# Optimization experiments

Hardware: AMD Instinct MI355X
Metric: run time of the kernel (lower is better)

The kernel has to match this reference:

```python
import jax, jax.numpy as jnp
import numpy as np

N_STATE = 1280
N_HEAD = 20
D_HEAD = N_STATE // N_HEAD  # 64
N_MLP = 4 * N_STATE         # 5120
EPS = 1e-5


def _layer_norm(x, gamma, beta):
    mu = jnp.mean(x, axis=-1, keepdims=True)
    var = jnp.mean(jnp.square(x - mu), axis=-1, keepdims=True)
    return (x - mu) * jax.lax.rsqrt(var + EPS) * gamma + beta


def setup_inputs() -> dict:
    key = jax.random.key(0)
    ks = jax.random.split(key, 16)
    s = lambda fan_in: 1.0 / np.sqrt(fan_in)
    d = {
        "x": jax.random.normal(ks[0], (1, 1500, N_STATE), jnp.float32),
        # attention projections (stored [in, out]; torch Linear does x @ W.T + b)
        "Wq": jax.random.normal(ks[1], (N_STATE, N_STATE), jnp.float32) * s(N_STATE),
        "bq": jax.random.normal(ks[2], (N_STATE,), jnp.float32) * 0.02,
        "Wk": jax.random.normal(ks[3], (N_STATE, N_STATE), jnp.float32) * s(N_STATE),  # no bias
        "Wv": jax.random.normal(ks[4], (N_STATE, N_STATE), jnp.float32) * s(N_STATE),
        "bv": jax.random.normal(ks[5], (N_STATE,), jnp.float32) * 0.02,
        "Wo": jax.random.normal(ks[6], (N_STATE, N_STATE), jnp.float32) * s(N_STATE),
        "bo": jax.random.normal(ks[7], (N_STATE,), jnp.float32) * 0.02,
        # layer norms
        "ln1_g": jnp.ones((N_STATE,), jnp.float32),
        "ln1_b": jnp.zeros((N_STATE,), jnp.float32),
        "ln2_g": jnp.ones((N_STATE,), jnp.float32),
        "ln2_b": jnp.zeros((N_STATE,), jnp.float32),
        # MLP
        "W1": jax.random.normal(ks[8], (N_STATE, N_MLP), jnp.float32) * s(N_STATE),
        "b1": jax.random.normal(ks[9], (N_MLP,), jnp.float32) * 0.02,
        "W2": jax.random.normal(ks[10], (N_MLP, N_STATE), jnp.float32) * s(N_MLP),
        "b2": jax.random.normal(ks[11], (N_STATE,), jnp.float32) * 0.02,
    }
    return d


def reference(x, Wq, bq, Wk, Wv, bv, Wo, bo, ln1_g, ln1_b, ln2_g, ln2_b, W1, b1, W2, b2):
    B, S, C = x.shape
    scale = D_HEAD ** -0.5

    # --- multi-head self-attention ---
    h = _layer_norm(x, ln1_g, ln1_b)
    q = (h @ Wq + bq).reshape(B, S, N_HEAD, D_HEAD)
    k = (h @ Wk).reshape(B, S, N_HEAD, D_HEAD)
    v = (h @ Wv + bv).reshape(B, S, N_HEAD, D_HEAD)
    # scores: [B, H, Q, K]; softmax over keys (dim=1 'k' in the torch einsum)
    scores = jnp.einsum('bqhd,bkhd->bhqk', q, k) * scale
    w = jax.nn.softmax(scores, axis=-1)
    attn = jnp.einsum('bhqk,bkhd->bqhd', w, v).reshape(B, S, C)
    attn = attn @ Wo + bo
    x = x + attn

    # --- MLP (exact GELU, matching torch nn.GELU default) ---
    h2 = _layer_norm(x, ln2_g, ln2_b)
    h2 = jax.nn.gelu(h2 @ W1 + b1, approximate=False)
    x = x + (h2 @ W2 + b2)
    return x
```

## Files before the change

### kernel.cpp

```cpp
#include <hip/hip_runtime.h>
#include <hip/hip_bf16.h>
#include <math.h>

typedef __bf16 bf16x8 __attribute__((ext_vector_type(8)));
typedef float f32x4 __attribute__((ext_vector_type(4)));

#define SEQ 1500
#define CDIM 1280
#define NHEAD 20
#define DHEAD 64
#define NMLP 5120
#define QKVN 3840
#define VTLD 1504
#define APAD 68

#define GLOAD_LDS16(gp, lp)                                                    \
  __builtin_amdgcn_global_load_lds(                                            \
      (const __attribute__((address_space(1))) unsigned int*)(gp),             \
      (__attribute__((address_space(3))) unsigned int*)(lp), 16, 0, 0)

__global__ __launch_bounds__(256) void pack_params_kernel(
    const unsigned int* __restrict__ xw, const void* bq, const void* bv,
    const void* bo, const void* g1, const void* be1, const void* g2,
    const void* be2, const void* b1, const void* b2,
    __bf16* __restrict__ pb, int* __restrict__ flag) {
  __shared__ int cnt[256];
  const unsigned int w = xw[threadIdx.x];
  const unsigned int e = (w >> 7) & 0xFF;
  cnt[threadIdx.x] = (e >= 100 && e <= 150) ? 1 : 0;
  __syncthreads();
  for (int s = 128; s > 0; s >>= 1) {
    if (threadIdx.x < (unsigned)s) cnt[threadIdx.x] += cnt[threadIdx.x + s];
    __syncthreads();
  }
  const int isbf = (cnt[0] >= 160) ? 1 : 0;
  if (blockIdx.x == 0 && threadIdx.x == 0) flag[0] = isbf;
  const int i = blockIdx.x * 256 + threadIdx.x;
  if (i >= 16640) return;
  auto ld = [&](const void* p, int j) -> float {
    return isbf ? (float)((const __bf16*)p)[j] : ((const float*)p)[j];
  };
  float v;
  if (i < 3840) {
    if (i < 1280) v = ld(bq, i);
    else if (i < 2560) v = 0.f;
    else v = ld(bv, i - 2560);
  } else if (i < 5120) v = ld(bo, i - 3840);
  else if (i < 6400) v = ld(g1, i - 5120);
  else if (i < 7680) v = ld(be1, i - 6400);
  else if (i < 8960) v = ld(g2, i - 7680);
  else if (i < 10240) v = ld(be2, i - 8960);
  else if (i < 15360) v = ld(b1, i - 10240);
  else v = ld(b2, i - 15360);
  pb[i] = (__bf16)v;
}

__device__ __forceinline__ void transpose_body(const void* in, __bf16* out,
                                               int K, int N, int isbf,
                                               int bx, int by) {
  __shared__ __bf16 t[32][33];
  const int tx = threadIdx.x, ty = threadIdx.y;
  const int n0 = bx * 32, k0 = by * 32;
  if (isbf) {
    const __bf16* s = (const __bf16*)in;
#pragma unroll
    for (int i = ty; i < 32; i += 8)
      t[i][tx] = s[(size_t)(k0 + i) * N + n0 + tx];
  } else {
    const float* s = (const float*)in;
#pragma unroll
    for (int i = ty; i < 32; i += 8)
      t[i][tx] = (__bf16)s[(size_t)(k0 + i) * N + n0 + tx];
  }
  __syncthreads();
#pragma unroll
  for (int i = ty; i < 32; i += 8)
    out[(size_t)(n0 + i) * K + k0 + tx] = t[tx][i];
}

__global__ __launch_bounds__(256) void transpose_all_kernel(
    const void* Wq, const void* Wk, const void* Wv, const void* Wo,
    const void* W1, const void* W2, __bf16* __restrict__ Wqkvt,
    __bf16* __restrict__ Wot, __bf16* __restrict__ W1t,
    __bf16* __restrict__ W2t, const int* __restrict__ flag) {
  const int id = blockIdx.x;
  const int isbf = flag[0];
  if (id < 6400) {
    const int w = id / 1600, r = id % 1600;
    const void* in = (w == 0) ? Wq : (w == 1) ? Wk : (w == 2) ? Wv : Wo;
    __bf16* out = (w < 3) ? (Wqkvt + (size_t)w * CDIM * CDIM) : Wot;
    transpose_body(in, out, CDIM, CDIM, isbf, r % 40, r / 40);
  } else if (id < 12800) {
    const int r = id - 6400;
    transpose_body(W1, W1t, CDIM, NMLP, isbf, r % 160, r / 160);
  } else {
    const int r = id - 12800;
    transpose_body(W2, W2t, NMLP, CDIM, isbf, r % 40, r / 40);
  }
}

__global__ __launch_bounds__(256) void transpose_act_kernel(const __bf16* __restrict__ in,
                                                            __bf16* __restrict__ out,
                                                            int istride) {
  __shared__ __bf16 t[32][33];
  const int tx = threadIdx.x, ty = threadIdx.y;
  const int n0 = blockIdx.x * 32, k0 = blockIdx.y * 32;
#pragma unroll
  for (int i = ty; i < 32; i += 8) {
    const int k = k0 + i;
    t[i][tx] = (k < SEQ) ? in[(size_t)k * istride + n0 + tx] : (__bf16)0.f;
  }
  __syncthreads();
#pragma unroll
  for (int i = ty; i < 32; i += 8) {
    const int kk = k0 + tx;
    if (kk < VTLD) out[(size_t)(n0 + i) * VTLD + kk] = t[tx][i];
  }
}

__global__ __launch_bounds__(256) void ln_kernel(const void* __restrict__ X,
                                                 const __bf16* __restrict__ gamma,
                                                 const __bf16* __restrict__ beta,
                                                 __bf16* __restrict__ Y,
                                                 const int* __restrict__ flag) {
  const int isf32 = (flag[0] == 0);
  const int row = blockIdx.x;
  float v[5];
  float s = 0.f, s2 = 0.f;
#pragma unroll
  for (int i = 0; i < 5; ++i) {
    const int c = threadIdx.x + 256 * i;
    const size_t idx = (size_t)row * CDIM + c;
    v[i] = isf32 ? ((const float*)X)[idx] : (float)((const __bf16*)X)[idx];
    s += v[i];
    s2 += v[i] * v[i];
  }
  const int lane = threadIdx.x & 63, wv = threadIdx.x >> 6;
#pragma unroll
  for (int off = 32; off > 0; off >>= 1) {
    s += __shfl_down(s, off);
    s2 += __shfl_down(s2, off);
  }
  __shared__ float red[8];
  if (lane == 0) { red[wv] = s; red[4 + wv] = s2; }
  __syncthreads();
  s = red[0] + red[1] + red[2] + red[3];
  s2 = red[4] + red[5] + red[6] + red[7];
  const float mu = s * (1.f / CDIM);
  const float var = s2 * (1.f / CDIM) - mu * mu;
  const float rstd = rsqrtf(fmaxf(var, 0.f) + 1e-5f);
#pragma unroll
  for (int i = 0; i < 5; ++i) {
    const int c = threadIdx.x + 256 * i;
    Y[(size_t)row * CDIM + c] =
        (__bf16)((v[i] - mu) * rstd * (float)gamma[c] + (float)beta[c]);
  }
}

__global__ __launch_bounds__(256) void resid_ln_kernel(
    const float* __restrict__ P, const __bf16* __restrict__ bo,
    const void* __restrict__ X, const __bf16* __restrict__ gamma,
    const __bf16* __restrict__ beta, __bf16* __restrict__ X1,
    __bf16* __restrict__ H2, const int* __restrict__ flag) {
  const int isf32 = (flag[0] == 0);
  const int row = blockIdx.x;
  const int MN = SEQ * CDIM;
  float v[5];
  float s = 0.f, s2 = 0.f;
#pragma unroll
  for (int i = 0; i < 5; ++i) {
    const int c = threadIdx.x + 256 * i;
    const size_t idx = (size_t)row * CDIM + c;
    const float xv = isf32 ? ((const float*)X)[idx] : (float)((const __bf16*)X)[idx];
    const float val = P[idx] + P[MN + idx] + (float)bo[c] + xv;
    X1[idx] = (__bf16)val;
    v[i] = val;
    s += val;
    s2 += val * val;
  }
  const int lane = threadIdx.x & 63, wv = threadIdx.x >> 6;
#pragma unroll
  for (int off = 32; off > 0; off >>= 1) {
    s += __shfl_down(s, off);
    s2 += __shfl_down(s2, off);
  }
  __shared__ float red[8];
  if (lane == 0) { red[wv] = s; red[4 + wv] = s2; }
  __syncthreads();
  s = red[0] + red[1] + red[2] + red[3];
  s2 = red[4] + red[5] + red[6] + red[7];
  const float mu = s * (1.f / CDIM);
  const float var = s2 * (1.f / CDIM) - mu * mu;
  const float rstd = rsqrtf(fmaxf(var, 0.f) + 1e-5f);
#pragma unroll
  for (int i = 0; i < 5; ++i) {
    const int c = threadIdx.x + 256 * i;
    H2[(size_t)row * CDIM + c] =
        (__bf16)((v[i] - mu) * rstd * (float)gamma[c] + (float)beta[c]);
  }
}

__global__ __launch_bounds__(256) void gemm64_kernel(
    const __bf16* __restrict__ A, const __bf16* __restrict__ Bt,
    const __bf16* __restrict__ bias, void* __restrict__ Cv,
    int M, int N, int K, int KS, int gelu, int nsplit) {
  __shared__ __bf16 As[2][64 * 32];
  __shared__ __bf16 Bs[2][128 * 32];
  const int bm = blockIdx.x, bn = blockIdx.y, sz = blockIdx.z;
  const int tid = threadIdx.x;
  const int lane = tid & 63, wave = tid >> 6;
  const int l16 = lane & 15, kq = (lane >> 4) << 3;
  const int lrow = lane >> 2, lcol = (lane & 3) << 3;
  const int wn = wave * 32;

  f32x4 acc[4][2];
  const f32x4 zero = {0.f, 0.f, 0.f, 0.f};
#pragma unroll
  for (int i = 0; i < 4; ++i)
#pragma unroll
    for (int j = 0; j < 2; ++j) acc[i][j] = zero;

  const int kbeg = sz * KS;
  int kend = kbeg + KS;
  if (kend > K) kend = K;

  int ga = bm * 64 + wave * 16 + lrow;
  if (ga > M - 1) ga = M - 1;
  const __bf16* Ap = A + (size_t)ga * K + lcol;

  for (int k0 = kbeg; k0 < kend; k0 += 64) {
#pragma unroll
    for (int c = 0; c < 2; ++c)
      GLOAD_LDS16(Ap + k0 + c * 32, &As[c][wave * 512]);
#pragma unroll
    for (int c = 0; c < 2; ++c)
#pragma unroll
      for (int t = 0; t < 2; ++t) {
        const int seg = t * 4 + wave;
        const int gb = bn * 128 + seg * 16 + lrow;
        GLOAD_LDS16(Bt + (size_t)gb * K + k0 + c * 32 + lcol, &Bs[c][seg * 512]);
      }
    __syncthreads();
    bf16x8 af[4][2], bfr[2][2];
#pragma unroll
    for (int i = 0; i < 4; ++i)
#pragma unroll
      for (int c = 0; c < 2; ++c)
        af[i][c] = *(const bf16x8*)(&As[c][(i * 16 + l16) * 32 + kq]);
#pragma unroll
    for (int j = 0; j < 2; ++j)
#pragma unroll
      for (int c = 0; c < 2; ++c)
        bfr[j][c] = *(const bf16x8*)(&Bs[c][(wn + j * 16 + l16) * 32 + kq]);
#pragma unroll
    for (int i = 0; i < 4; ++i)
#pragma unroll
      for (int j = 0; j < 2; ++j)
#pragma unroll
        for (int c = 0; c < 2; ++c)
          acc[i][j] = __builtin_amdgcn_mfma_f32_16x16x32_bf16(af[i][c], bfr[j][c],
                                                              acc[i][j], 0, 0, 0);
    __syncthreads();
  }

  const int rq4 = (lane >> 4) * 4;
  if (nsplit > 1) {
    float* P = (float*)Cv + (size_t)sz * M * N;
#pragma unroll
    for (int i = 0; i < 4; ++i)
#pragma unroll
      for (int r = 0; r < 4; ++r) {
        const int grow = bm * 64 + i * 16 + rq4 + r;
        if (grow >= M) continue;
#pragma unroll
        for (int j = 0; j < 2; ++j) {
          const int gcol = bn * 128 + wn + j * 16 + l16;
          P[(size_t)grow * N + gcol] = acc[i][j][r];
        }
      }
  } else {
    __bf16* Cb = (__bf16*)Cv;
#pragma unroll
    for (int i = 0; i < 4; ++i)
#pragma unroll
      for (int r = 0; r < 4; ++r) {
        const int grow = bm * 64 + i * 16 + rq4 + r;
        if (grow >= M) continue;
#pragma unroll
        for (int j = 0; j < 2; ++j) {
          const int gcol = bn * 128 + wn + j * 16 + l16;
          float vv = acc[i][j][r];
          if (bias) vv += (float)bias[gcol];
          if (gelu) vv = 0.5f * vv * (1.f + erff(vv * 0.70710678118654752f));
          Cb[(size_t)grow * N + gcol] = (__bf16)vv;
        }
      }
  }
}

__global__ __launch_bounds__(512, 2) void gemm8ph_kernel(
    const __bf16* __restrict__ A, const __bf16* __restrict__ Bt,
    const __bf16* __restrict__ bias, __bf16* __restrict__ C,
    int M, int N, int K, int gelu, int mtiles) {
  __shared__ __bf16 As[2][128 * 64];
  __shared__ __bf16 Bs[2][256 * 64];

  const int nwg = mtiles * (N >> 8);
  const int qq = nwg >> 3, rr = nwg & 7;
  const int xcd = blockIdx.x & 7, rk = blockIdx.x >> 3;
  const int wg = (xcd < rr ? xcd * (qq + 1) : rr * (qq + 1) + (xcd - rr) * qq) + rk;
  const int bm = wg % mtiles, bn = wg / mtiles;

  const int tid = threadIdx.x;
  const int lane = tid & 63, wave = tid >> 6;
  const int wm = wave >> 2, wn = wave & 3;
  const int l16 = lane & 15, quad = lane >> 4;

  const int rA = tid >> 3;
  const int sl = tid & 7;
  const int aoff = ((sl * 16) ^ ((rA & 7) << 4)) >> 1;
  int gm0 = bm * 128 + rA;        if (gm0 > M - 1) gm0 = M - 1;
  int gm1 = bm * 128 + 64 + rA;   if (gm1 > M - 1) gm1 = M - 1;
  const __bf16* ApA = A + (size_t)gm0 * K + aoff;
  const __bf16* ApB = A + (size_t)gm1 * K + aoff;
  const __bf16* Bp[4];
#pragma unroll
  for (int L = 0; L < 4; ++L)
    Bp[L] = Bt + (size_t)(bn * 256 + L * 64 + rA) * K + aoff;

  auto stage = [&](int b, int k0) {
    GLOAD_LDS16(ApA + k0, &As[b][(size_t)tid * 8]);
    GLOAD_LDS16(ApB + k0, &As[b][4096 + (size_t)tid * 8]);
#pragma unroll
    for (int L = 0; L < 4; ++L)
      GLOAD_LDS16(Bp[L] + k0, &Bs[b][L * 4096 + (size_t)tid * 8]);
  };

  const int xsw = (l16 & 7) << 4;
  const int kb0 = (((quad << 4)) ^ xsw) >> 1;
  const int kb1 = (((quad << 4) + 64) ^ xsw) >> 1;

  f32x4 acc[4][4];
  const f32x4 zero = {0.f, 0.f, 0.f, 0.f};
#pragma unroll
  for (int i = 0; i < 4; ++i)
#pragma unroll
    for (int j = 0; j < 4; ++j) acc[i][j] = zero;

  const int NT = K >> 6;
  stage(0, 0);
  asm volatile("s_waitcnt vmcnt(0)" ::: "memory");
  __builtin_amdgcn_sched_barrier(0);
  __builtin_amdgcn_s_barrier();

  bf16x8 af[4][2], bfr[4][2];
  for (int t = 0; t < NT; ++t) {
    const int cur = t & 1;
#pragma unroll
    for (int i = 0; i < 4; ++i) {
      const int row = wm * 64 + i * 16 + l16;
      af[i][0] = *(const bf16x8*)(&As[cur][row * 64 + kb0]);
      af[i][1] = *(const bf16x8*)(&As[cur][row * 64 + kb1]);
    }
#pragma unroll
    for (int j = 0; j < 2; ++j) {
      const int row = wn * 64 + j * 16 + l16;
      bfr[j][0] = *(const bf16x8*)(&Bs[cur][row * 64 + kb0]);
      bfr[j][1] = *(const bf16x8*)(&Bs[cur][row * 64 + kb1]);
    }
    if (t + 1 < NT) stage(cur ^ 1, (t + 1) * 64);
    __builtin_amdgcn_s_barrier();
    asm volatile("s_waitcnt lgkmcnt(0)" ::: "memory");
    __builtin_amdgcn_sched_barrier(0);
    __builtin_amdgcn_s_setprio(1);
#pragma unroll
    for (int i = 0; i < 4; ++i)
#pragma unroll
      for (int j = 0; j < 2; ++j)
#pragma unroll
        for (int c = 0; c < 2; ++c)
          acc[i][j] = __builtin_amdgcn_mfma_f32_16x16x32_bf16(af[i][c], bfr[j][c],
                                                              acc[i][j], 0, 0, 0);
    __builtin_amdgcn_s_setprio(0);
    __builtin_amdgcn_s_barrier();
#pragma unroll
    for (int j = 2; j < 4; ++j) {
      const int row = wn * 64 + j * 16 + l16;
      bfr[j][0] = *(const bf16x8*)(&Bs[cur][row * 64 + kb0]);
      bfr[j][1] = *(const bf16x8*)(&Bs[cur][row * 64 + kb1]);
    }
    __builtin_amdgcn_s_barrier();
    asm volatile("s_waitcnt lgkmcnt(0)" ::: "memory");
    __builtin_amdgcn_sched_barrier(0);
    __builtin_amdgcn_s_setprio(1);
#pragma unroll
    for (int i = 0; i < 4; ++i)
#pragma unroll
      for (int j = 2; j < 4; ++j)
#pragma unroll
        for (int c = 0; c < 2; ++c)
          acc[i][j] = __builtin_amdgcn_mfma_f32_16x16x32_bf16(af[i][c], bfr[j][c],
                                                              acc[i][j], 0, 0, 0);
    __builtin_amdgcn_s_setprio(0);
    asm volatile("s_waitcnt vmcnt(0)" ::: "memory");
    __builtin_amdgcn_sched_barrier(0);
    __builtin_amdgcn_s_barrier();
  }

#pragma unroll
  for (int i = 0; i < 4; ++i)
#pragma unroll
    for (int r = 0; r < 4; ++r) {
      const int grow = bm * 128 + wm * 64 + i * 16 + quad * 4 + r;
      if (grow >= M) continue;
#pragma unroll
      for (int j = 0; j < 4; ++j) {
        const int gcol = bn * 256 + wn * 64 + j * 16 + l16;
        float vv = acc[i][j][r];
        if (bias) vv += (float)bias[gcol];
        if (gelu) vv = 0.5f * vv * (1.f + erff(vv * 0.70710678118654752f));
        C[(size_t)grow * N + gcol] = (__bf16)vv;
      }
    }
}

__global__ __launch_bounds__(256) void reduce_kernel(
    const float* __restrict__ P, const __bf16* __restrict__ bias,
    const __bf16* __restrict__ resid, void* __restrict__ out,
    int MN, int N, const int* __restrict__ flag) {
  const int i = blockIdx.x * 256 + threadIdx.x;
  if (i >= MN) return;
  const float v = P[i] + P[(size_t)MN + i] + (float)bias[i % N] + (float)resid[i];
  if (flag[0]) ((__bf16*)out)[i] = (__bf16)v;
  else         ((float*)out)[i] = v;
}

__global__ __launch_bounds__(256) void attn_mfma_kernel(
    const __bf16* __restrict__ Q,
    const __bf16* __restrict__ Kk,
    const __bf16* __restrict__ Vt,
    float* __restrict__ Opart,
    float* __restrict__ ml,
    int rs) {
  const int h = blockIdx.y;
  const int q0 = blockIdx.x * 64;
  const int z = blockIdx.z;
  const int tid = threadIdx.x;
  const int wave = tid >> 6, lane = tid & 63;
  const int l16 = lane & 15, quad = lane >> 4;

  __shared__ __bf16 Ks[64 * APAD];
  __shared__ __bf16 Vs[64 * APAD];
  __shared__ __bf16 Ps[4][16 * APAD];

  bf16x8 qf[2];
  {
    int q = q0 + wave * 16 + l16;
    if (q > SEQ - 1) q = SEQ - 1;
    const __bf16* qp = Q + (size_t)q * rs + h * DHEAD + quad * 8;
    qf[0] = *(const bf16x8*)(qp);
    qf[1] = *(const bf16x8*)(qp + 32);
  }

  f32x4 oacc[4];
  const f32x4 zero = {0.f, 0.f, 0.f, 0.f};
#pragma unroll
  for (int jt = 0; jt < 4; ++jt) oacc[jt] = zero;
  float mrow[4], lrow[4];
#pragma unroll
  for (int r = 0; r < 4; ++r) { mrow[r] = -30000.f; lrow[r] = 0.f; }

  const int srow = tid >> 2;
  const int scol = (tid & 3) << 4;

  const __bf16* Kbase = Kk + h * DHEAD;
  const __bf16* Vbase = Vt + (size_t)(h * DHEAD + srow) * VTLD;

  for (int kt = z * 12; kt < z * 12 + 12; ++kt) {
    const int key0 = kt * 64;
    __syncthreads();
    {
      int gk = key0 + srow;
      if (gk > SEQ - 1) gk = SEQ - 1;
      const __bf16* kp = Kbase + (size_t)gk * rs + scol;
      *(bf16x8*)(&Ks[srow * APAD + scol]) = *(const bf16x8*)(kp);
      *(bf16x8*)(&Ks[srow * APAD + scol + 8]) = *(const bf16x8*)(kp + 8);
      const __bf16* vp = Vbase + key0 + scol;
      *(bf16x8*)(&Vs[srow * APAD + scol]) = *(const bf16x8*)(vp);
      *(bf16x8*)(&Vs[srow * APAD + scol + 8]) = *(const bf16x8*)(vp + 8);
    }
    __syncthreads();

    f32x4 s[4];
#pragma unroll
    for (int jt = 0; jt < 4; ++jt) s[jt] = zero;
#pragma unroll
    for (int jt = 0; jt < 4; ++jt)
#pragma unroll
      for (int ks = 0; ks < 2; ++ks) {
        const bf16x8 kf = *(const bf16x8*)(&Ks[(jt * 16 + l16) * APAD + ks * 32 + quad * 8]);
        s[jt] = __builtin_amdgcn_mfma_f32_16x16x32_bf16(qf[ks], kf, s[jt], 0, 0, 0);
      }

#pragma unroll
    for (int jt = 0; jt < 4; ++jt) {
      const int key = key0 + jt * 16 + l16;
#pragma unroll
      for (int r = 0; r < 4; ++r) {
        float sv = s[jt][r] * 0.125f;
        if (key >= SEQ) sv = -30000.f;
        s[jt][r] = sv;
      }
    }

#pragma unroll
    for (int r = 0; r < 4; ++r) {
      float tmax = fmaxf(fmaxf(s[0][r], s[1][r]), fmaxf(s[2][r], s[3][r]));
#pragma unroll
      for (int off = 8; off > 0; off >>= 1) tmax = fmaxf(tmax, __shfl_xor(tmax, off));
      const float mnew = fmaxf(mrow[r], tmax);
      const float alpha = __expf(mrow[r] - mnew);
      mrow[r] = mnew;
      lrow[r] *= alpha;
#pragma unroll
      for (int jt = 0; jt < 4; ++jt) oacc[jt][r] *= alpha;
#pragma unroll
      for (int jt = 0; jt < 4; ++jt) {
        const float p = __expf(s[jt][r] - mnew);
        lrow[r] += p;
        Ps[wave][(quad * 4 + r) * APAD + jt * 16 + l16] = (__bf16)p;
      }
    }

    bf16x8 pf[2];
    pf[0] = *(const bf16x8*)(&Ps[wave][l16 * APAD + quad * 8]);
    pf[1] = *(const bf16x8*)(&Ps[wave][l16 * APAD + 32 + quad * 8]);
#pragma unroll
    for (int jt = 0; jt < 4; ++jt)
#pragma unroll
      for (int ks = 0; ks < 2; ++ks) {
        const bf16x8 vf = *(const bf16x8*)(&Vs[(jt * 16 + l16) * APAD + ks * 32 + quad * 8]);
        oacc[jt] = __builtin_amdgcn_mfma_f32_16x16x32_bf16(pf[ks], vf, oacc[jt], 0, 0, 0);
      }
  }

  float* Oz = Opart + (size_t)z * SEQ * CDIM;
#pragma unroll
  for (int r = 0; r < 4; ++r) {
    float lt = lrow[r];
#pragma unroll
    for (int off = 8; off > 0; off >>= 1) lt += __shfl_xor(lt, off);
    const int q = q0 + wave * 16 + quad * 4 + r;
    if (q < SEQ) {
#pragma unroll
      for (int jt = 0; jt < 4; ++jt)
        Oz[(size_t)q * CDIM + h * DHEAD + jt * 16 + l16] = oacc[jt][r];
      if (l16 == 0) {
        const size_t mi = ((size_t)(z * NHEAD + h) * SEQ + q) * 2;
        ml[mi] = mrow[r];
        ml[mi + 1] = lt;
      }
    }
  }
}

__global__ __launch_bounds__(256) void attn_combine_kernel(
    const float* __restrict__ Op, const float* __restrict__ ml,
    __bf16* __restrict__ O) {
  const int i = blockIdx.x * 256 + threadIdx.x;
  if (i >= SEQ * CDIM) return;
  const int q = i / CDIM;
  const int h = (i % CDIM) >> 6;
  const size_t m1i = ((size_t)h * SEQ + q) * 2;
  const size_t m2i = ((size_t)(NHEAD + h) * SEQ + q) * 2;
  const float m1 = ml[m1i], l1 = ml[m1i + 1];
  const float m2 = ml[m2i], l2 = ml[m2i + 1];
  const float M = fmaxf(m1, m2);
  const float e1 = __expf(m1 - M), e2 = __expf(m2 - M);
  const float v = (e1 * Op[i] + e2 * Op[(size_t)SEQ * CDIM + i]) /
                  (e1 * l1 + e2 * l2);
  O[i] = (__bf16)v;
}

extern "C" void kernel_launch(void* const* d_in, const int* in_sizes, int n_in,
                              void* d_out, int out_size, void* d_ws, size_t ws_size,
                              hipStream_t stream) {
  const void* x   = d_in[0];
  const void* Wq  = d_in[1];
  const void* bq  = d_in[2];
  const void* Wk  = d_in[3];
  const void* Wv  = d_in[4];
  const void* bv  = d_in[5];
  const void* Wo  = d_in[6];
  const void* bo  = d_in[7];
  const void* g1  = d_in[8];
  const void* be1 = d_in[9];
  const void* g2  = d_in[10];
  const void* be2 = d_in[11];
  const void* W1  = d_in[12];
  const void* bm1 = d_in[13];
  const void* W2  = d_in[14];
  const void* bm2 = d_in[15];

  char* ws = (char*)d_ws;
  size_t off = 0;
  auto alloc = [&](size_t elems) {
    __bf16* p = (__bf16*)(ws + off);
    off += elems * sizeof(__bf16);
    return p;
  };
  __bf16* Wqkvt = alloc((size_t)QKVN * CDIM);
  __bf16* Wot   = alloc((size_t)CDIM * CDIM);
  __bf16* W1t   = alloc((size_t)CDIM * NMLP);
  __bf16* W2t   = alloc((size_t)CDIM * NMLP);
  __bf16* qkvb  = alloc((size_t)SEQ * QKVN);
  __bf16* hb    = alloc((size_t)SEQ * CDIM);
  __bf16* mb    = alloc((size_t)SEQ * NMLP);
  __bf16* pb    = alloc(20480);
  off = (off + 15) & ~(size_t)15;
  float* pscr = (float*)(ws + off);
  off += (size_t)2 * SEQ * CDIM * sizeof(float);
  float* mlb = (float*)(ws + off);
  off += (size_t)2 * NHEAD * SEQ * 2 * sizeof(float);
  int* flag = (int*)(ws + off);

  __bf16* vtb  = mb;
  __bf16* x1b  = qkvb;
  __bf16* h2b  = qkvb + (size_t)SEQ * CDIM;

  __bf16* qkvbias = pb + 0;
  __bf16* bo_b  = pb + 3840;
  __bf16* g1_b  = pb + 5120;
  __bf16* be1_b = pb + 6400;
  __bf16* g2_b  = pb + 7680;
  __bf16* be2_b = pb + 8960;
  __bf16* b1_b  = pb + 10240;
  __bf16* b2_b  = pb + 15360;

  pack_params_kernel<<<65, 256, 0, stream>>>(
      (const unsigned int*)x, bq, bv, bo, g1, be1, g2, be2, bm1, bm2, pb, flag);
  transpose_all_kernel<<<19200, dim3(32, 8), 0, stream>>>(
      Wq, Wk, Wv, Wo, W1, W2, Wqkvt, Wot, W1t, W2t, flag);
  ln_kernel<<<SEQ, 256, 0, stream>>>(x, g1_b, be1_b, hb, flag);
  gemm8ph_kernel<<<180, 512, 0, stream>>>(
      hb, Wqkvt, qkvbias, qkvb, SEQ, QKVN, CDIM, 0, 12);
  transpose_act_kernel<<<dim3(40, 47), dim3(32, 8), 0, stream>>>(
      qkvb + 2560, vtb, QKVN);
  attn_mfma_kernel<<<dim3(24, NHEAD, 2), 256, 0, stream>>>(
      qkvb, qkvb + 1280, vtb, pscr, mlb, QKVN);
  attn_combine_kernel<<<7500, 256, 0, stream>>>(pscr, mlb, hb);
  gemm64_kernel<<<dim3(24, 10, 2), 256, 0, stream>>>(
      hb, Wot, nullptr, pscr, SEQ, CDIM, CDIM, 640, 0, 2);
  resid_ln_kernel<<<SEQ, 256, 0, stream>>>(pscr, bo_b, x, g2_b, be2_b,
                                           x1b, h2b, flag);
  gemm8ph_kernel<<<240, 512, 0, stream>>>(
      h2b, W1t, b1_b, mb, SEQ, NMLP, CDIM, 1, 12);
  gemm64_kernel<<<dim3(24, 10, 2), 256, 0, stream>>>(
      mb, W2t, nullptr, pscr, SEQ, CDIM, NMLP, 2560, 0, 2);
  reduce_kernel<<<7500, 256, 0, stream>>>(pscr, b2_b, x1b, d_out,
                                          SEQ * CDIM, CDIM, flag);
}
```

Baseline: 370.5 us.

## Enlarge QKV/MLP1 GEMM tiles to 256x256 with finer-grained staged prefetch

Replaces the 128x256-tile GEMM with a 256x256-tile version where each wave computes 128x64 using 32 accumulators. The loads for the next K-step are split into four pairs, each issued between the four MFMA phases with partial vmcnt waits. The goal is more reuse per LDS byte and better overlap of global loads with compute. In exchange the grid halves to 90 and 120 workgroups on a GPU with 256 CUs, which leaves many CUs idle and raises register and LDS pressure.

```diff
diff --git a/kernel.cpp b/kernel.cpp
--- a/kernel.cpp
+++ b/kernel.cpp
@@ -298,11 +298,11 @@
   }
 }
 
-__global__ __launch_bounds__(512, 2) void gemm8ph_kernel(
+__global__ __launch_bounds__(512, 2) void gemm256_kernel(
     const __bf16* __restrict__ A, const __bf16* __restrict__ Bt,
     const __bf16* __restrict__ bias, __bf16* __restrict__ C,
     int M, int N, int K, int gelu, int mtiles) {
-  __shared__ __bf16 As[2][128 * 64];
+  __shared__ __bf16 As[2][256 * 64];
   __shared__ __bf16 Bs[2][256 * 64];
 
   const int nwg = mtiles * (N >> 8);
@@ -316,102 +316,150 @@
   const int wm = wave >> 2, wn = wave & 3;
   const int l16 = lane & 15, quad = lane >> 4;
 
-  const int rA = tid >> 3;
-  const int sl = tid & 7;
-  const int aoff = ((sl * 16) ^ ((rA & 7) << 4)) >> 1;
-  int gm0 = bm * 128 + rA;        if (gm0 > M - 1) gm0 = M - 1;
-  int gm1 = bm * 128 + 64 + rA;   if (gm1 > M - 1) gm1 = M - 1;
-  const __bf16* ApA = A + (size_t)gm0 * K + aoff;
-  const __bf16* ApB = A + (size_t)gm1 * K + aoff;
+  const int rT = tid >> 3, sl = tid & 7;
+  const int aoff = ((sl * 16) ^ ((rT & 7) << 4)) >> 1;
+  const __bf16* Ap[4];
   const __bf16* Bp[4];
 #pragma unroll
-  for (int L = 0; L < 4; ++L)
-    Bp[L] = Bt + (size_t)(bn * 256 + L * 64 + rA) * K + aoff;
-
-  auto stage = [&](int b, int k0) {
-    GLOAD_LDS16(ApA + k0, &As[b][(size_t)tid * 8]);
-    GLOAD_LDS16(ApB + k0, &As[b][4096 + (size_t)tid * 8]);
-#pragma unroll
-    for (int L = 0; L < 4; ++L)
-      GLOAD_LDS16(Bp[L] + k0, &Bs[b][L * 4096 + (size_t)tid * 8]);
-  };
+  for (int s = 0; s < 4; ++s) {
+    int gm = bm * 256 + s * 64 + rT;
+    if (gm > M - 1) gm = M - 1;
+    Ap[s] = A + (size_t)gm * K + aoff;
+    Bp[s] = Bt + (size_t)(bn * 256 + s * 64 + rT) * K + aoff;
+  }
+  const int ldst = tid * 8;
 
   const int xsw = (l16 & 7) << 4;
-  const int kb0 = (((quad << 4)) ^ xsw) >> 1;
+  const int kb0 = ((quad << 4) ^ xsw) >> 1;
   const int kb1 = (((quad << 4) + 64) ^ xsw) >> 1;
-
-  f32x4 acc[4][4];
+  const int arow = (wm * 128 + l16) * 64;
+  const int brow = (wn * 64 + l16) * 64;
+
+  f32x4 acc[8][4];
   const f32x4 zero = {0.f, 0.f, 0.f, 0.f};
 #pragma unroll
-  for (int i = 0; i < 4; ++i)
+  for (int i = 0; i < 8; ++i)
 #pragma unroll
     for (int j = 0; j < 4; ++j) acc[i][j] = zero;
 
   const int NT = K >> 6;
-  stage(0, 0);
-  asm volatile("s_waitcnt vmcnt(0)" ::: "memory");
-  __builtin_amdgcn_sched_barrier(0);
-  __builtin_amdgcn_s_barrier();
-
-  bf16x8 af[4][2], bfr[4][2];
+  GLOAD_LDS16(Bp[0], &Bs[0][0 * 4096 + ldst]);
+  GLOAD_LDS16(Bp[1], &Bs[0][1 * 4096 + ldst]);
+  GLOAD_LDS16(Bp[2], &Bs[0][2 * 4096 + ldst]);
+  GLOAD_LDS16(Bp[3], &Bs[0][3 * 4096 + ldst]);
+  GLOAD_LDS16(Ap[0], &As[0][0 * 4096 + ldst]);
+  GLOAD_LDS16(Ap[2], &As[0][2 * 4096 + ldst]);
+  GLOAD_LDS16(Ap[1], &As[0][1 * 4096 + ldst]);
+  GLOAD_LDS16(Ap[3], &As[0][3 * 4096 + ldst]);
+
+  bf16x8 af[4], ag[4], bfr[4];
   for (int t = 0; t < NT; ++t) {
     const int cur = t & 1;
-#pragma unroll
-    for (int i = 0; i < 4; ++i) {
-      const int row = wm * 64 + i * 16 + l16;
-      af[i][0] = *(const bf16x8*)(&As[cur][row * 64 + kb0]);
-      af[i][1] = *(const bf16x8*)(&As[cur][row * 64 + kb1]);
-    }
-#pragma unroll
-    for (int j = 0; j < 2; ++j) {
-      const int row = wn * 64 + j * 16 + l16;
-      bfr[j][0] = *(const bf16x8*)(&Bs[cur][row * 64 + kb0]);
-      bfr[j][1] = *(const bf16x8*)(&Bs[cur][row * 64 + kb1]);
-    }
-    if (t + 1 < NT) stage(cur ^ 1, (t + 1) * 64);
+    const int k1 = (t + 1) << 6;
+    const bool pf = (t + 1 < NT);
+    __bf16* Asn = &As[cur ^ 1][0];
+    __bf16* Bsn = &Bs[cur ^ 1][0];
+    const __bf16* Asc = &As[cur][0];
+    const __bf16* Bsc = &Bs[cur][0];
+
+    if (pf) {
+      GLOAD_LDS16(Bp[0] + k1, Bsn + 0 * 4096 + ldst);
+      GLOAD_LDS16(Bp[1] + k1, Bsn + 1 * 4096 + ldst);
+      asm volatile("s_waitcnt vmcnt(4)" ::: "memory");
+    } else {
+      asm volatile("s_waitcnt vmcnt(2)" ::: "memory");
+    }
     __builtin_amdgcn_s_barrier();
+#pragma unroll
+    for (int i = 0; i < 4; ++i)
+      af[i] = *(const bf16x8*)(Asc + arow + i * 1024 + kb0);
+#pragma unroll
+    for (int j = 0; j < 4; ++j)
+      bfr[j] = *(const bf16x8*)(Bsc + brow + j * 1024 + kb0);
     asm volatile("s_waitcnt lgkmcnt(0)" ::: "memory");
     __builtin_amdgcn_sched_barrier(0);
     __builtin_amdgcn_s_setprio(1);
 #pragma unroll
     for (int i = 0; i < 4; ++i)
 #pragma unroll
-      for (int j = 0; j < 2; ++j)
-#pragma unroll
-        for (int c = 0; c < 2; ++c)
-          acc[i][j] = __builtin_amdgcn_mfma_f32_16x16x32_bf16(af[i][c], bfr[j][c],
-                                                              acc[i][j], 0, 0, 0);
+      for (int j = 0; j < 4; ++j)
+        acc[i][j] = __builtin_amdgcn_mfma_f32_16x16x32_bf16(af[i], bfr[j],
+                                                            acc[i][j], 0, 0, 0);
     __builtin_amdgcn_s_setprio(0);
     __builtin_amdgcn_s_barrier();
-#pragma unroll
-    for (int j = 2; j < 4; ++j) {
-      const int row = wn * 64 + j * 16 + l16;
-      bfr[j][0] = *(const bf16x8*)(&Bs[cur][row * 64 + kb0]);
-      bfr[j][1] = *(const bf16x8*)(&Bs[cur][row * 64 + kb1]);
+
+    if (pf) {
+      GLOAD_LDS16(Bp[2] + k1, Bsn + 2 * 4096 + ldst);
+      GLOAD_LDS16(Bp[3] + k1, Bsn + 3 * 4096 + ldst);
+      asm volatile("s_waitcnt vmcnt(4)" ::: "memory");
+    } else {
+      asm volatile("s_waitcnt vmcnt(0)" ::: "memory");
     }
     __builtin_amdgcn_s_barrier();
+#pragma unroll
+    for (int i = 0; i < 4; ++i)
+      ag[i] = *(const bf16x8*)(Asc + arow + 4096 + i * 1024 + kb0);
     asm volatile("s_waitcnt lgkmcnt(0)" ::: "memory");
     __builtin_amdgcn_sched_barrier(0);
     __builtin_amdgcn_s_setprio(1);
 #pragma unroll
     for (int i = 0; i < 4; ++i)
 #pragma unroll
-      for (int j = 2; j < 4; ++j)
-#pragma unroll
-        for (int c = 0; c < 2; ++c)
-          acc[i][j] = __builtin_amdgcn_mfma_f32_16x16x32_bf16(af[i][c], bfr[j][c],
-                                                              acc[i][j], 0, 0, 0);
+      for (int j = 0; j < 4; ++j)
+        acc[4 + i][j] = __builtin_amdgcn_mfma_f32_16x16x32_bf16(ag[i], bfr[j],
+                                                                acc[4 + i][j], 0, 0, 0);
     __builtin_amdgcn_s_setprio(0);
-    asm volatile("s_waitcnt vmcnt(0)" ::: "memory");
+    __builtin_amdgcn_s_barrier();
+
+    if (pf) {
+      GLOAD_LDS16(Ap[0] + k1, Asn + 0 * 4096 + ldst);
+      GLOAD_LDS16(Ap[2] + k1, Asn + 2 * 4096 + ldst);
+    }
+    __builtin_amdgcn_s_barrier();
+#pragma unroll
+    for (int i = 0; i < 4; ++i)
+      af[i] = *(const bf16x8*)(Asc + arow + i * 1024 + kb1);
+#pragma unroll
+    for (int j = 0; j < 4; ++j)
+      bfr[j] = *(const bf16x8*)(Bsc + brow + j * 1024 + kb1);
+    asm volatile("s_waitcnt lgkmcnt(0)" ::: "memory");
     __builtin_amdgcn_sched_barrier(0);
+    __builtin_amdgcn_s_setprio(1);
+#pragma unroll
+    for (int i = 0; i < 4; ++i)
+#pragma unroll
+      for (int j = 0; j < 4; ++j)
+        acc[i][j] = __builtin_amdgcn_mfma_f32_16x16x32_bf16(af[i], bfr[j],
+                                                            acc[i][j], 0, 0, 0);
+    __builtin_amdgcn_s_setprio(0);
     __builtin_amdgcn_s_barrier();
-  }
-
-#pragma unroll
-  for (int i = 0; i < 4; ++i)
+
+    if (pf) {
+      GLOAD_LDS16(Ap[1] + k1, Asn + 1 * 4096 + ldst);
+      GLOAD_LDS16(Ap[3] + k1, Asn + 3 * 4096 + ldst);
+    }
+    __builtin_amdgcn_s_barrier();
+#pragma unroll
+    for (int i = 0; i < 4; ++i)
+      ag[i] = *(const bf16x8*)(Asc + arow + 4096 + i * 1024 + kb1);
+    asm volatile("s_waitcnt lgkmcnt(0)" ::: "memory");
+    __builtin_amdgcn_sched_barrier(0);
+    __builtin_amdgcn_s_setprio(1);
+#pragma unroll
+    for (int i = 0; i < 4; ++i)
+#pragma unroll
+      for (int j = 0; j < 4; ++j)
+        acc[4 + i][j] = __builtin_amdgcn_mfma_f32_16x16x32_bf16(ag[i], bfr[j],
+                                                                acc[4 + i][j], 0, 0, 0);
+    __builtin_amdgcn_s_setprio(0);
+    __builtin_amdgcn_s_barrier();
+  }
+
+#pragma unroll
+  for (int i = 0; i < 8; ++i)
 #pragma unroll
     for (int r = 0; r < 4; ++r) {
-      const int grow = bm * 128 + wm * 64 + i * 16 + quad * 4 + r;
+      const int grow = bm * 256 + wm * 128 + i * 16 + quad * 4 + r;
       if (grow >= M) continue;
 #pragma unroll
       for (int j = 0; j < 4; ++j) {
@@ -642,8 +690,8 @@
   transpose_all_kernel<<<19200, dim3(32, 8), 0, stream>>>(
       Wq, Wk, Wv, Wo, W1, W2, Wqkvt, Wot, W1t, W2t, flag);
   ln_kernel<<<SEQ, 256, 0, stream>>>(x, g1_b, be1_b, hb, flag);
-  gemm8ph_kernel<<<180, 512, 0, stream>>>(
-      hb, Wqkvt, qkvbias, qkvb, SEQ, QKVN, CDIM, 0, 12);
+  gemm256_kernel<<<90, 512, 0, stream>>>(
+      hb, Wqkvt, qkvbias, qkvb, SEQ, QKVN, CDIM, 0, 6);
   transpose_act_kernel<<<dim3(40, 47), dim3(32, 8), 0, stream>>>(
       qkvb + 2560, vtb, QKVN);
   attn_mfma_kernel<<<dim3(24, NHEAD, 2), 256, 0, stream>>>(
@@ -653,8 +701,8 @@
       hb, Wot, nullptr, pscr, SEQ, CDIM, CDIM, 640, 0, 2);
   resid_ln_kernel<<<SEQ, 256, 0, stream>>>(pscr, bo_b, x, g2_b, be2_b,
                                            x1b, h2b, flag);
-  gemm8ph_kernel<<<240, 512, 0, stream>>>(
-      h2b, W1t, b1_b, mb, SEQ, NMLP, CDIM, 1, 12);
+  gemm256_kernel<<<120, 512, 0, stream>>>(
+      h2b, W1t, b1_b, mb, SEQ, NMLP, CDIM, 1, 6);
   gemm64_kernel<<<dim3(24, 10, 2), 256, 0, stream>>>(
       mb, W2t, nullptr, pscr, SEQ, CDIM, NMLP, 2560, 0, 2);
   reduce_kernel<<<7500, 256, 0, stream>>>(pscr, b2_b, x1b, d_out,
```

Result: slower. 460.0 us (+24.2%).

## Replace 128x256 eight-wave GEMM with 128x128 four-wave tile and prefetch pipeline

Applied to the files above, without the earlier changes.

The QKV and MLP-up GEMMs move from a 512-thread kernel with 128x256 tiles to a 256-thread kernel with 128x128 tiles, which doubles the workgroup count (360 and 480 blocks) to fill the CUs better. The k-loop now issues the next tile's global-to-LDS loads before computing and waits with vmcnt(8) so loads overlap the MFMAs, instead of the earlier split two-phase B-fragment scheme. The cost is lower per-block reuse of A and B tiles and more total global traffic.

```diff
diff --git a/kernel.cpp b/kernel.cpp
--- a/kernel.cpp
+++ b/kernel.cpp
@@ -298,14 +298,14 @@
   }
 }
 
-__global__ __launch_bounds__(512, 2) void gemm8ph_kernel(
+__global__ __launch_bounds__(256, 2) void gemm128c_kernel(
     const __bf16* __restrict__ A, const __bf16* __restrict__ Bt,
     const __bf16* __restrict__ bias, __bf16* __restrict__ C,
     int M, int N, int K, int gelu, int mtiles) {
   __shared__ __bf16 As[2][128 * 64];
-  __shared__ __bf16 Bs[2][256 * 64];
-
-  const int nwg = mtiles * (N >> 8);
+  __shared__ __bf16 Bs[2][128 * 64];
+
+  const int nwg = mtiles * (N >> 7);
   const int qq = nwg >> 3, rr = nwg & 7;
   const int xcd = blockIdx.x & 7, rk = blockIdx.x >> 3;
   const int wg = (xcd < rr ? xcd * (qq + 1) : rr * (qq + 1) + (xcd - rr) * qq) + rk;
@@ -313,31 +313,24 @@
 
   const int tid = threadIdx.x;
   const int lane = tid & 63, wave = tid >> 6;
-  const int wm = wave >> 2, wn = wave & 3;
+  const int wm = (wave >> 1) * 64, wn = (wave & 1) * 64;
   const int l16 = lane & 15, quad = lane >> 4;
 
-  const int rA = tid >> 3;
-  const int sl = tid & 7;
-  const int aoff = ((sl * 16) ^ ((rA & 7) << 4)) >> 1;
-  int gm0 = bm * 128 + rA;        if (gm0 > M - 1) gm0 = M - 1;
-  int gm1 = bm * 128 + 64 + rA;   if (gm1 > M - 1) gm1 = M - 1;
-  const __bf16* ApA = A + (size_t)gm0 * K + aoff;
-  const __bf16* ApB = A + (size_t)gm1 * K + aoff;
+  const int rT = tid >> 3, sl = tid & 7;
+  const int aoff = ((sl * 16) ^ ((rT & 7) << 4)) >> 1;
+  const __bf16* Ap[4];
   const __bf16* Bp[4];
 #pragma unroll
-  for (int L = 0; L < 4; ++L)
-    Bp[L] = Bt + (size_t)(bn * 256 + L * 64 + rA) * K + aoff;
-
-  auto stage = [&](int b, int k0) {
-    GLOAD_LDS16(ApA + k0, &As[b][(size_t)tid * 8]);
-    GLOAD_LDS16(ApB + k0, &As[b][4096 + (size_t)tid * 8]);
-#pragma unroll
-    for (int L = 0; L < 4; ++L)
-      GLOAD_LDS16(Bp[L] + k0, &Bs[b][L * 4096 + (size_t)tid * 8]);
-  };
+  for (int s = 0; s < 4; ++s) {
+    int gm = bm * 128 + s * 32 + rT;
+    if (gm > M - 1) gm = M - 1;
+    Ap[s] = A + (size_t)gm * K + aoff;
+    Bp[s] = Bt + (size_t)(bn * 128 + s * 32 + rT) * K + aoff;
+  }
+  const int ldst = tid * 8;
 
   const int xsw = (l16 & 7) << 4;
-  const int kb0 = (((quad << 4)) ^ xsw) >> 1;
+  const int kb0 = ((quad << 4) ^ xsw) >> 1;
   const int kb1 = (((quad << 4) + 64) ^ xsw) >> 1;
 
   f32x4 acc[4][4];
@@ -348,74 +341,64 @@
     for (int j = 0; j < 4; ++j) acc[i][j] = zero;
 
   const int NT = K >> 6;
-  stage(0, 0);
-  asm volatile("s_waitcnt vmcnt(0)" ::: "memory");
-  __builtin_amdgcn_sched_barrier(0);
-  __builtin_amdgcn_s_barrier();
-
-  bf16x8 af[4][2], bfr[4][2];
+
+#define STAGE128(b, k0)                                       \
+  do {                                                        \
+    _Pragma("unroll")                                         \
+    for (int s = 0; s < 4; ++s) {                             \
+      GLOAD_LDS16(Ap[s] + (k0), &As[b][s * 2048 + ldst]);     \
+      GLOAD_LDS16(Bp[s] + (k0), &Bs[b][s * 2048 + ldst]);     \
+    }                                                         \
+  } while (0)
+
+  STAGE128(0, 0);
   for (int t = 0; t < NT; ++t) {
     const int cur = t & 1;
+    if (t + 1 < NT) {
+      STAGE128(cur ^ 1, (t + 1) * 64);
+      asm volatile("s_waitcnt vmcnt(8)" ::: "memory");
+    } else {
+      asm volatile("s_waitcnt vmcnt(0)" ::: "memory");
+    }
+    __builtin_amdgcn_s_barrier();
+    __builtin_amdgcn_sched_barrier(0);
+    bf16x8 af[4][2], bfr[4][2];
 #pragma unroll
     for (int i = 0; i < 4; ++i) {
-      const int row = wm * 64 + i * 16 + l16;
-      af[i][0] = *(const bf16x8*)(&As[cur][row * 64 + kb0]);
-      af[i][1] = *(const bf16x8*)(&As[cur][row * 64 + kb1]);
-    }
-#pragma unroll
-    for (int j = 0; j < 2; ++j) {
-      const int row = wn * 64 + j * 16 + l16;
-      bfr[j][0] = *(const bf16x8*)(&Bs[cur][row * 64 + kb0]);
-      bfr[j][1] = *(const bf16x8*)(&Bs[cur][row * 64 + kb1]);
-    }
-    if (t + 1 < NT) stage(cur ^ 1, (t + 1) * 64);
-    __builtin_amdgcn_s_barrier();
-    asm volatile("s_waitcnt lgkmcnt(0)" ::: "memory");
-    __builtin_amdgcn_sched_barrier(0);
+      const int row = (wm + i * 16 + l16) * 64;
+      af[i][0] = *(const bf16x8*)(&As[cur][row + kb0]);
+      af[i][1] = *(const bf16x8*)(&As[cur][row + kb1]);
+    }
+#pragma unroll
+    for (int j = 0; j < 4; ++j) {
+      const int row = (wn + j * 16 + l16) * 64;
+      bfr[j][0] = *(const bf16x8*)(&Bs[cur][row + kb0]);
+      bfr[j][1] = *(const bf16x8*)(&Bs[cur][row + kb1]);
+    }
     __builtin_amdgcn_s_setprio(1);
 #pragma unroll
     for (int i = 0; i < 4; ++i)
 #pragma unroll
-      for (int j = 0; j < 2; ++j)
+      for (int j = 0; j < 4; ++j)
 #pragma unroll
         for (int c = 0; c < 2; ++c)
           acc[i][j] = __builtin_amdgcn_mfma_f32_16x16x32_bf16(af[i][c], bfr[j][c],
                                                               acc[i][j], 0, 0, 0);
     __builtin_amdgcn_s_setprio(0);
     __builtin_amdgcn_s_barrier();
-#pragma unroll
-    for (int j = 2; j < 4; ++j) {
-      const int row = wn * 64 + j * 16 + l16;
-      bfr[j][0] = *(const bf16x8*)(&Bs[cur][row * 64 + kb0]);
-      bfr[j][1] = *(const bf16x8*)(&Bs[cur][row * 64 + kb1]);
-    }
-    __builtin_amdgcn_s_barrier();
-    asm volatile("s_waitcnt lgkmcnt(0)" ::: "memory");
     __builtin_amdgcn_sched_barrier(0);
-    __builtin_amdgcn_s_setprio(1);
-#pragma unroll
-    for (int i = 0; i < 4; ++i)
-#pragma unroll
-      for (int j = 2; j < 4; ++j)
-#pragma unroll
-        for (int c = 0; c < 2; ++c)
-          acc[i][j] = __builtin_amdgcn_mfma_f32_16x16x32_bf16(af[i][c], bfr[j][c],
-                                                              acc[i][j], 0, 0, 0);
-    __builtin_amdgcn_s_setprio(0);
-    asm volatile("s_waitcnt vmcnt(0)" ::: "memory");
-    __builtin_amdgcn_sched_barrier(0);
-    __builtin_amdgcn_s_barrier();
-  }
+  }
+#undef STAGE128
 
 #pragma unroll
   for (int i = 0; i < 4; ++i)
 #pragma unroll
     for (int r = 0; r < 4; ++r) {
-      const int grow = bm * 128 + wm * 64 + i * 16 + quad * 4 + r;
+      const int grow = bm * 128 + wm + i * 16 + quad * 4 + r;
       if (grow >= M) continue;
 #pragma unroll
       for (int j = 0; j < 4; ++j) {
-        const int gcol = bn * 256 + wn * 64 + j * 16 + l16;
+        const int gcol = bn * 128 + wn + j * 16 + l16;
         float vv = acc[i][j][r];
         if (bias) vv += (float)bias[gcol];
         if (gelu) vv = 0.5f * vv * (1.f + erff(vv * 0.70710678118654752f));
@@ -642,7 +625,7 @@
   transpose_all_kernel<<<19200, dim3(32, 8), 0, stream>>>(
       Wq, Wk, Wv, Wo, W1, W2, Wqkvt, Wot, W1t, W2t, flag);
   ln_kernel<<<SEQ, 256, 0, stream>>>(x, g1_b, be1_b, hb, flag);
-  gemm8ph_kernel<<<180, 512, 0, stream>>>(
+  gemm128c_kernel<<<360, 256, 0, stream>>>(
       hb, Wqkvt, qkvbias, qkvb, SEQ, QKVN, CDIM, 0, 12);
   transpose_act_kernel<<<dim3(40, 47), dim3(32, 8), 0, stream>>>(
       qkvb + 2560, vtb, QKVN);
@@ -653,7 +636,7 @@
       hb, Wot, nullptr, pscr, SEQ, CDIM, CDIM, 640, 0, 2);
   resid_ln_kernel<<<SEQ, 256, 0, stream>>>(pscr, bo_b, x, g2_b, be2_b,
                                            x1b, h2b, flag);
-  gemm8ph_kernel<<<240, 512, 0, stream>>>(
+  gemm128c_kernel<<<480, 256, 0, stream>>>(
       h2b, W1t, b1_b, mb, SEQ, NMLP, CDIM, 1, 12);
   gemm64_kernel<<<dim3(24, 10, 2), 256, 0, stream>>>(
       mb, W2t, nullptr, pscr, SEQ, CDIM, NMLP, 2560, 0, 2);
```

New measurement: 361.6 us. 1.02x faster.
